# Optimization experiments

Measured on AMD Instinct MI355X. Metric: run time of the kernel, lower is better.

## Reference

```python
import jax, jax.numpy as jnp
import numpy as np

N = 8192
E = 262144
DIN = 512
DOUT = 256


def setup_inputs() -> dict:
    key = jax.random.key(0)
    k1, k2, k3, k4 = jax.random.split(key, 4)
    x = jax.random.normal(k1, (N, DIN), dtype=jnp.float32)
    edge_index = jax.random.randint(k2, (2, E), 0, N, dtype=jnp.int64)
    edge_weight = jax.random.uniform(k3, (E,), dtype=jnp.float32)
    W = jax.random.normal(k4, (DOUT, DIN), dtype=jnp.float32) * (1.0 / np.sqrt(DIN))
    return {"x": x, "edge_index": edge_index, "edge_weight": edge_weight, "W": W}


def reference(x, edge_index, edge_weight, W):
    n = x.shape[0]
    # Linear(dim_in, dim_out, bias=False): h = x @ W.T  -> [N, DOUT]
    h = x @ W.T
    # Dense adjacency: A[src, dst] += w (to_dense_adj sums duplicate edges)
    src, dst = edge_index[0], edge_index[1]
    A = jnp.zeros((n, n), dtype=x.dtype).at[src, dst].add(edge_weight)
    # degree from A BEFORE self-loops, then +1 from the added eye on degree_matrix
    deg = jnp.sum(A, axis=1) + 1.0
    # sqrt(inverse(diag(deg))) == diag(1/sqrt(deg)); apply as row scaling
    dinv_sqrt = 1.0 / jnp.sqrt(deg)  # [N]
    A = A + jnp.eye(n, dtype=x.dtype)  # self-loops on adjacency
    # x = D^{-1/2} @ (A.T @ (D^{-1/2} @ h))
    h = dinv_sqrt[:, None] * h
    h = A.T @ h
    h = dinv_sqrt[:, None] * h
    return h
```

## Files before the change

### kernel.cpp

```cpp
#include <hip/hip_runtime.h>

static constexpr int DIN = 512;
static constexpr int DOUT = 256;
static constexpr int CAP = 128;
static constexpr int EPT = 8;
static constexpr float DEG_SCALE = 1048576.0f;
static constexpr float DEG_INV = 1.0f / 1048576.0f;

typedef __attribute__((ext_vector_type(8))) short short8;
typedef __attribute__((ext_vector_type(4))) float f32x4;
typedef __attribute__((ext_vector_type(2))) unsigned int u32x2;
typedef __attribute__((ext_vector_type(4))) unsigned int u32x4;

__device__ inline unsigned short f2bf(float f) {
  unsigned int b = __float_as_uint(f);
  unsigned int r = (b + 0x7fffu + ((b >> 16) & 1u)) >> 16;
  return (unsigned short)r;
}
__device__ inline float bf_lo(unsigned int packed) { return __uint_as_float(packed << 16); }
__device__ inline float bf_hi(unsigned int packed) { return __uint_as_float(packed & 0xffff0000u); }

__device__ inline short8 cvt8(const f32x4 a, const f32x4 b) {
  short8 o;
  o[0] = (short)f2bf(a[0]); o[1] = (short)f2bf(a[1]);
  o[2] = (short)f2bf(a[2]); o[3] = (short)f2bf(a[3]);
  o[4] = (short)f2bf(b[0]); o[5] = (short)f2bf(b[1]);
  o[6] = (short)f2bf(b[2]); o[7] = (short)f2bf(b[3]);
  return o;
}

__global__ __launch_bounds__(256) void k_prep(
    const float* __restrict__ W, unsigned short* __restrict__ wbb,
    int* __restrict__ dz, int n2, int wgroups) {
  const int gid = blockIdx.x * 256 + threadIdx.x;
  if (gid < n2) dz[gid] = 0;
  const int wi = gid - n2;
  if (wi >= 0 && wi < wgroups) {
    const f32x4* src = (const f32x4*)(W + (size_t)wi * 8);
    f32x4 a = src[0], b = src[1];
    *(short8*)(wbb + (size_t)wi * 8) = cvt8(a, b);
  }
}

__global__ __launch_bounds__(256) void k_deg(
    const int* __restrict__ ei, const float* __restrict__ ew,
    int* __restrict__ degi, int E) {
  const int e0 = blockIdx.x * 256 * EPT + threadIdx.x;
  int sv[EPT], wq[EPT];
#pragma unroll
  for (int u = 0; u < EPT; ++u) {
    const int e = e0 + u * 256;
    sv[u] = __builtin_nontemporal_load(ei + e);
    wq[u] = __float2int_rn(__builtin_nontemporal_load(ew + e) * DEG_SCALE);
  }
#pragma unroll
  for (int u = 0; u < EPT; ++u) atomicAdd(&degi[sv[u]], wq[u]);
}

__global__ __launch_bounds__(256) void k_bin(
    const int* __restrict__ ei, const float* __restrict__ ew,
    int* __restrict__ cursor, uint2* __restrict__ bucket, int E) {
  const int e = blockIdx.x * 256 + threadIdx.x;
  if (e >= E) return;
  int srcv = __builtin_nontemporal_load(ei + e);
  int dstv = __builtin_nontemporal_load(ei + E + e);
  float w = __builtin_nontemporal_load(ew + e);
  int pos = atomicAdd(&cursor[dstv], 1);
  if (pos < CAP) {
    u32x2 v;
    v[0] = (unsigned)srcv;
    v[1] = __float_as_uint(w);
    __builtin_nontemporal_store(v, (u32x2*)(bucket + (size_t)dstv * CAP + pos));
  }
}

__global__ __launch_bounds__(256) void k_gemm(
    const float* __restrict__ x, const unsigned short* __restrict__ wbb,
    unsigned short* __restrict__ h1b) {
  const int lane = threadIdx.x & 63;
  const int wv = threadIdx.x >> 6;
  const int bm = blockIdx.x * 16;
  const int colb = wv * 64;
  const int r = lane & 15;
  const int kg = lane >> 4;
  f32x4 acc[4] = {};
  const float* arow = x + (size_t)(bm + r) * DIN + kg * 8;
  const unsigned short* brow0 = wbb + (size_t)(colb + r) * DIN + kg * 8;
#pragma unroll
  for (int k0 = 0; k0 < DIN; k0 += 32) {
    f32x4 a0 = *(const f32x4*)(arow + k0);
    f32x4 a1 = *(const f32x4*)(arow + k0 + 4);
    short8 av = cvt8(a0, a1);
#pragma unroll
    for (int nt = 0; nt < 4; ++nt) {
      short8 bv = *(const short8*)(brow0 + (size_t)nt * 16 * DIN + k0);
      acc[nt] = __builtin_amdgcn_mfma_f32_16x16x32_bf16(av, bv, acc[nt], 0, 0, 0);
    }
  }
#pragma unroll
  for (int i = 0; i < 4; ++i) {
    int row = bm + kg * 4 + i;
#pragma unroll
    for (int nt = 0; nt < 4; ++nt) {
      h1b[(size_t)row * DOUT + colb + nt * 16 + r] = f2bf(acc[nt][i]);
    }
  }
}

__global__ __launch_bounds__(256, 4) void k_gather(
    const unsigned short* __restrict__ h1b, const int* __restrict__ degi,
    const int* __restrict__ cursor, const uint2* __restrict__ bucket,
    float* __restrict__ out) {
  const int lane = threadIdx.x & 63;
  const int wv = threadIdx.x >> 6;
  const int dst = blockIdx.x * 4 + wv;
  const int cl = lane & 31;
  const int half = lane >> 5;
  const int cnt = min(cursor[dst], CAP);

  const u32x4 selfv = *(const u32x4*)(h1b + (size_t)dst * DOUT + cl * 8);
  const float sd = __frsqrt_rn(1.0f + (float)degi[dst] * DEG_INV);

  float acc[8] = {};

  for (int base = 0; base < cnt; base += 64) {
    const int c = min(64, cnt - base);
    int sv = 0;
    float wl = 0.f;
    if (lane < c) {
      u32x2 ev = __builtin_nontemporal_load(
          (const u32x2*)(bucket + (size_t)dst * CAP + base + lane));
      sv = (int)ev[0];
      wl = __uint_as_float(ev[1]) *
           __frsqrt_rn(1.0f + (float)degi[sv] * DEG_INV);
    }
    const int npair = ((c + 15) >> 4) << 3;
    for (int j = 0; j < npair; j += 8) {
      u32x4 rbuf[8];
#pragma unroll
      for (int u = 0; u < 8; ++u) {
        int src = __shfl(sv, 2 * (j + u) + half);
        rbuf[u] = *(const u32x4*)(h1b + (size_t)src * DOUT + cl * 8);
      }
#pragma unroll
      for (int u = 0; u < 8; ++u) {
        float w = __shfl(wl, 2 * (j + u) + half);
        acc[0] = fmaf(w, bf_lo(rbuf[u][0]), acc[0]);
        acc[1] = fmaf(w, bf_hi(rbuf[u][0]), acc[1]);
        acc[2] = fmaf(w, bf_lo(rbuf[u][1]), acc[2]);
        acc[3] = fmaf(w, bf_hi(rbuf[u][1]), acc[3]);
        acc[4] = fmaf(w, bf_lo(rbuf[u][2]), acc[4]);
        acc[5] = fmaf(w, bf_hi(rbuf[u][2]), acc[5]);
        acc[6] = fmaf(w, bf_lo(rbuf[u][3]), acc[6]);
        acc[7] = fmaf(w, bf_hi(rbuf[u][3]), acc[7]);
      }
    }
  }

#pragma unroll
  for (int k = 0; k < 8; ++k) acc[k] += __shfl_xor(acc[k], 32);

  if (half == 0) {
    f32x4 o0v, o1v;
    o0v[0] = sd * fmaf(sd, bf_lo(selfv[0]), acc[0]);
    o0v[1] = sd * fmaf(sd, bf_hi(selfv[0]), acc[1]);
    o0v[2] = sd * fmaf(sd, bf_lo(selfv[1]), acc[2]);
    o0v[3] = sd * fmaf(sd, bf_hi(selfv[1]), acc[3]);
    o1v[0] = sd * fmaf(sd, bf_lo(selfv[2]), acc[4]);
    o1v[1] = sd * fmaf(sd, bf_hi(selfv[2]), acc[5]);
    o1v[2] = sd * fmaf(sd, bf_lo(selfv[3]), acc[6]);
    o1v[3] = sd * fmaf(sd, bf_hi(selfv[3]), acc[7]);
    float* op = out + (size_t)dst * DOUT + cl * 8;
    __builtin_nontemporal_store(o0v, (f32x4*)op);
    __builtin_nontemporal_store(o1v, (f32x4*)(op + 4));
  }
}

extern "C" void kernel_launch(void* const* d_in, const int* in_sizes, int n_in,
                              void* d_out, int out_size, void* d_ws, size_t ws_size,
                              hipStream_t stream) {
  const float* x = (const float*)d_in[0];
  const int* ei = (const int*)d_in[1];
  const float* ew = (const float*)d_in[2];
  const float* W = (const float*)d_in[3];
  float* out = (float*)d_out;

  const int n = in_sizes[0] / DIN;
  const int E = in_sizes[2];

  char* p = (char*)d_ws;
  auto alloc = [&](size_t bytes) {
    char* q = p;
    p += (bytes + 255) & ~(size_t)255;
    return q;
  };
  unsigned short* h1b = (unsigned short*)alloc((size_t)n * DOUT * 2);
  unsigned short* wbb = (unsigned short*)alloc((size_t)DOUT * DIN * 2);
  int* degi    = (int*)alloc((size_t)n * 4 * 2);
  int* cursor  = degi + n;
  uint2* bucket = (uint2*)alloc((size_t)n * CAP * 8);

  const int n2 = 2 * n;
  const int wgroups = DOUT * DIN / 8;
  const int prep_blocks = (n2 + wgroups + 255) / 256;

  k_prep<<<prep_blocks, 256, 0, stream>>>(W, wbb, degi, n2, wgroups);
  k_deg<<<E / (256 * EPT), 256, 0, stream>>>(ei, ew, degi, E);
  k_bin<<<(E + 255) / 256, 256, 0, stream>>>(ei, ew, cursor, bucket, E);
  k_gemm<<<n / 16, 256, 0, stream>>>(x, wbb, h1b);
  k_gather<<<n / 4, 256, 0, stream>>>(h1b, degi, cursor, bucket, out);
}
```

Baseline: 81.01 us.

## Replicate degree and bucket counters per XCD and fuse edge kernels

Merges the degree and binning kernels into one edge pass. Atomic counters and bucket slots are replicated per XCD, with the XCD read from a hardware register, so atomics stay within one die's L2 and avoid cross-die contention. Inverse-sqrt degrees are precomputed once inside the GEMM kernel, and the gather merges the per-XCD bucket segments through a prefix sum. The risk is a per-XCD cap of 24 slots, which could drop edges for a skewed in-degree, plus extra replicas to zero and sum.

```diff
diff --git a/kernel.cpp b/kernel.cpp
--- a/kernel.cpp
+++ b/kernel.cpp
@@ -2,8 +2,9 @@
 
 static constexpr int DIN = 512;
 static constexpr int DOUT = 256;
-static constexpr int CAP = 128;
-static constexpr int EPT = 8;
+static constexpr int NR = 8;
+static constexpr int SLOT = 24;
+static constexpr int EPT = 4;
 static constexpr float DEG_SCALE = 1048576.0f;
 static constexpr float DEG_INV = 1.0f / 1048576.0f;
 
@@ -29,12 +30,18 @@
   return o;
 }
 
+__device__ inline int xcd_id() {
+  int v;
+  asm volatile("s_getreg_b32 %0, hwreg(20)" : "=s"(v));
+  return v & (NR - 1);
+}
+
 __global__ __launch_bounds__(256) void k_prep(
     const float* __restrict__ W, unsigned short* __restrict__ wbb,
-    int* __restrict__ dz, int n2, int wgroups) {
+    int* __restrict__ dz, int nz, int wgroups) {
   const int gid = blockIdx.x * 256 + threadIdx.x;
-  if (gid < n2) dz[gid] = 0;
-  const int wi = gid - n2;
+  if (gid < nz) dz[gid] = 0;
+  const int wi = gid - nz;
   if (wi >= 0 && wi < wgroups) {
     const f32x4* src = (const f32x4*)(W + (size_t)wi * 8);
     f32x4 a = src[0], b = src[1];
@@ -42,41 +49,55 @@
   }
 }
 
-__global__ __launch_bounds__(256) void k_deg(
+__global__ __launch_bounds__(256) void k_edges(
     const int* __restrict__ ei, const float* __restrict__ ew,
-    int* __restrict__ degi, int E) {
+    int* __restrict__ degi_rep, int* __restrict__ cursor_rep,
+    uint2* __restrict__ bucket, int n, int E) {
+  const int x = xcd_id();
+  int* __restrict__ degr = degi_rep + (size_t)x * n;
+  int* __restrict__ curr = cursor_rep + (size_t)x * n;
   const int e0 = blockIdx.x * 256 * EPT + threadIdx.x;
-  int sv[EPT], wq[EPT];
+  int sv[EPT], dv[EPT], wq[EPT];
+  float wf[EPT];
 #pragma unroll
   for (int u = 0; u < EPT; ++u) {
-    const int e = e0 + u * 256;
+    const int e = min(e0 + u * 256, E - 1);
     sv[u] = __builtin_nontemporal_load(ei + e);
-    wq[u] = __float2int_rn(__builtin_nontemporal_load(ew + e) * DEG_SCALE);
-  }
-#pragma unroll
-  for (int u = 0; u < EPT; ++u) atomicAdd(&degi[sv[u]], wq[u]);
-}
-
-__global__ __launch_bounds__(256) void k_bin(
-    const int* __restrict__ ei, const float* __restrict__ ew,
-    int* __restrict__ cursor, uint2* __restrict__ bucket, int E) {
-  const int e = blockIdx.x * 256 + threadIdx.x;
-  if (e >= E) return;
-  int srcv = __builtin_nontemporal_load(ei + e);
-  int dstv = __builtin_nontemporal_load(ei + E + e);
-  float w = __builtin_nontemporal_load(ew + e);
-  int pos = atomicAdd(&cursor[dstv], 1);
-  if (pos < CAP) {
-    u32x2 v;
-    v[0] = (unsigned)srcv;
-    v[1] = __float_as_uint(w);
-    __builtin_nontemporal_store(v, (u32x2*)(bucket + (size_t)dstv * CAP + pos));
+    dv[u] = __builtin_nontemporal_load(ei + E + e);
+    wf[u] = __builtin_nontemporal_load(ew + e);
+    wq[u] = __float2int_rn(wf[u] * DEG_SCALE);
+  }
+  const bool live = (e0 + (EPT - 1) * 256) < E;
+#pragma unroll
+  for (int u = 0; u < EPT; ++u)
+    if (live || e0 + u * 256 < E) atomicAdd(&degr[sv[u]], wq[u]);
+  int pos[EPT];
+#pragma unroll
+  for (int u = 0; u < EPT; ++u)
+    pos[u] = (live || e0 + u * 256 < E) ? atomicAdd(&curr[dv[u]], 1) : SLOT;
+#pragma unroll
+  for (int u = 0; u < EPT; ++u) {
+    if (pos[u] < SLOT) {
+      u32x2 v;
+      v[0] = (unsigned)sv[u];
+      v[1] = __float_as_uint(wf[u]);
+      __builtin_nontemporal_store(
+          v, (u32x2*)(bucket + ((size_t)dv[u] * NR + x) * SLOT + pos[u]));
+    }
   }
 }
 
 __global__ __launch_bounds__(256) void k_gemm(
     const float* __restrict__ x, const unsigned short* __restrict__ wbb,
-    unsigned short* __restrict__ h1b) {
+    const int* __restrict__ degi_rep, float* __restrict__ sdeg,
+    unsigned short* __restrict__ h1b, int n) {
+  if (blockIdx.x < (n >> 8)) {
+    const int i = blockIdx.x * 256 + threadIdx.x;
+    int sum = 0;
+#pragma unroll
+    for (int r = 0; r < NR; ++r) sum += degi_rep[(size_t)r * n + i];
+    sdeg[i] = __frsqrt_rn(1.0f + (float)sum * DEG_INV);
+  }
   const int lane = threadIdx.x & 63;
   const int wv = threadIdx.x >> 6;
   const int bm = blockIdx.x * 16;
@@ -108,18 +129,26 @@
 }
 
 __global__ __launch_bounds__(256, 4) void k_gather(
-    const unsigned short* __restrict__ h1b, const int* __restrict__ degi,
-    const int* __restrict__ cursor, const uint2* __restrict__ bucket,
-    float* __restrict__ out) {
+    const unsigned short* __restrict__ h1b, const float* __restrict__ sdeg,
+    const int* __restrict__ cursor_rep, const uint2* __restrict__ bucket,
+    float* __restrict__ out, int n) {
   const int lane = threadIdx.x & 63;
   const int wv = threadIdx.x >> 6;
   const int dst = blockIdx.x * 4 + wv;
   const int cl = lane & 31;
   const int half = lane >> 5;
-  const int cnt = min(cursor[dst], CAP);
+
+  int pre[NR + 1];
+  pre[0] = 0;
+#pragma unroll
+  for (int r = 0; r < NR; ++r) {
+    int c = min(cursor_rep[(size_t)r * n + dst], SLOT);
+    pre[r + 1] = pre[r] + c;
+  }
+  const int cnt = pre[NR];
 
   const u32x4 selfv = *(const u32x4*)(h1b + (size_t)dst * DOUT + cl * 8);
-  const float sd = __frsqrt_rn(1.0f + (float)degi[dst] * DEG_INV);
+  const float sd = sdeg[dst];
 
   float acc[8] = {};
 
@@ -128,11 +157,15 @@
     int sv = 0;
     float wl = 0.f;
     if (lane < c) {
+      const int g = base + lane;
+      int rr = 0;
+#pragma unroll
+      for (int r = 1; r < NR; ++r) rr += (g >= pre[r]) ? 1 : 0;
+      const int slot = g - pre[rr];
       u32x2 ev = __builtin_nontemporal_load(
-          (const u32x2*)(bucket + (size_t)dst * CAP + base + lane));
+          (const u32x2*)(bucket + ((size_t)dst * NR + rr) * SLOT + slot));
       sv = (int)ev[0];
-      wl = __uint_as_float(ev[1]) *
-           __frsqrt_rn(1.0f + (float)degi[sv] * DEG_INV);
+      wl = __uint_as_float(ev[1]) * sdeg[sv];
     }
     const int npair = ((c + 15) >> 4) << 3;
     for (int j = 0; j < npair; j += 8) {
@@ -196,17 +229,18 @@
   };
   unsigned short* h1b = (unsigned short*)alloc((size_t)n * DOUT * 2);
   unsigned short* wbb = (unsigned short*)alloc((size_t)DOUT * DIN * 2);
-  int* degi    = (int*)alloc((size_t)n * 4 * 2);
-  int* cursor  = degi + n;
-  uint2* bucket = (uint2*)alloc((size_t)n * CAP * 8);
-
-  const int n2 = 2 * n;
+  int* degi_rep   = (int*)alloc((size_t)NR * n * 4);
+  int* cursor_rep = (int*)alloc((size_t)NR * n * 4);
+  float* sdeg     = (float*)alloc((size_t)n * 4);
+  uint2* bucket   = (uint2*)alloc((size_t)n * NR * SLOT * 8);
+
+  const int nz = 2 * NR * n;
   const int wgroups = DOUT * DIN / 8;
-  const int prep_blocks = (n2 + wgroups + 255) / 256;
-
-  k_prep<<<prep_blocks, 256, 0, stream>>>(W, wbb, degi, n2, wgroups);
-  k_deg<<<E / (256 * EPT), 256, 0, stream>>>(ei, ew, degi, E);
-  k_bin<<<(E + 255) / 256, 256, 0, stream>>>(ei, ew, cursor, bucket, E);
-  k_gemm<<<n / 16, 256, 0, stream>>>(x, wbb, h1b);
-  k_gather<<<n / 4, 256, 0, stream>>>(h1b, degi, cursor, bucket, out);
-}
+  const int prep_blocks = (nz + wgroups + 255) / 256;
+  const int edge_blocks = (E + 256 * EPT - 1) / (256 * EPT);
+
+  k_prep<<<prep_blocks, 256, 0, stream>>>(W, wbb, degi_rep, nz, wgroups);
+  k_edges<<<edge_blocks, 256, 0, stream>>>(ei, ew, degi_rep, cursor_rep, bucket, n, E);
+  k_gemm<<<n / 16, 256, 0, stream>>>(x, wbb, degi_rep, sdeg, h1b, n);
+  k_gather<<<n / 4, 256, 0, stream>>>(h1b, sdeg, cursor_rep, bucket, out, n);
+}
```

Result: faster. 77.12 us (-4.8%).

## Fuse degree, binning and GEMM kernels into one block-partitioned launch

Applied to the files above, without the earlier changes.

Merges the degree-atomic kernel, the edge-binning kernel and the bf16 MFMA GEMM into one launch whose block index picks the role. The independent stages can then run at the same time on the GPU, and two launch gaps disappear. It also changes edges per thread (degree 8→4, binning 1→2) and batches the cursor atomics in the binning path. The risk is heterogeneous blocks competing for resources and uneven scheduling. The binning path also drops its E bounds check, so it relies on E being a multiple of 512.

```diff
diff --git a/kernel.cpp b/kernel.cpp
--- a/kernel.cpp
+++ b/kernel.cpp
@@ -3,7 +3,8 @@
 static constexpr int DIN = 512;
 static constexpr int DOUT = 256;
 static constexpr int CAP = 128;
-static constexpr int EPT = 8;
+static constexpr int DEPT = 4;
+static constexpr int BEPT = 2;
 static constexpr float DEG_SCALE = 1048576.0f;
 static constexpr float DEG_INV = 1.0f / 1048576.0f;
 
@@ -31,10 +32,10 @@
 
 __global__ __launch_bounds__(256) void k_prep(
     const float* __restrict__ W, unsigned short* __restrict__ wbb,
-    int* __restrict__ dz, int n2, int wgroups) {
+    int* __restrict__ dz, int nz, int wgroups) {
   const int gid = blockIdx.x * 256 + threadIdx.x;
-  if (gid < n2) dz[gid] = 0;
-  const int wi = gid - n2;
+  if (gid < nz) dz[gid] = 0;
+  const int wi = gid - nz;
   if (wi >= 0 && wi < wgroups) {
     const f32x4* src = (const f32x4*)(W + (size_t)wi * 8);
     f32x4 a = src[0], b = src[1];
@@ -42,44 +43,57 @@
   }
 }
 
-__global__ __launch_bounds__(256) void k_deg(
+__global__ __launch_bounds__(256) void k_mid(
     const int* __restrict__ ei, const float* __restrict__ ew,
-    int* __restrict__ degi, int E) {
-  const int e0 = blockIdx.x * 256 * EPT + threadIdx.x;
-  int sv[EPT], wq[EPT];
-#pragma unroll
-  for (int u = 0; u < EPT; ++u) {
-    const int e = e0 + u * 256;
-    sv[u] = __builtin_nontemporal_load(ei + e);
-    wq[u] = __float2int_rn(__builtin_nontemporal_load(ew + e) * DEG_SCALE);
-  }
-#pragma unroll
-  for (int u = 0; u < EPT; ++u) atomicAdd(&degi[sv[u]], wq[u]);
-}
-
-__global__ __launch_bounds__(256) void k_bin(
-    const int* __restrict__ ei, const float* __restrict__ ew,
-    int* __restrict__ cursor, uint2* __restrict__ bucket, int E) {
-  const int e = blockIdx.x * 256 + threadIdx.x;
-  if (e >= E) return;
-  int srcv = __builtin_nontemporal_load(ei + e);
-  int dstv = __builtin_nontemporal_load(ei + E + e);
-  float w = __builtin_nontemporal_load(ew + e);
-  int pos = atomicAdd(&cursor[dstv], 1);
-  if (pos < CAP) {
-    u32x2 v;
-    v[0] = (unsigned)srcv;
-    v[1] = __float_as_uint(w);
-    __builtin_nontemporal_store(v, (u32x2*)(bucket + (size_t)dstv * CAP + pos));
-  }
-}
-
-__global__ __launch_bounds__(256) void k_gemm(
     const float* __restrict__ x, const unsigned short* __restrict__ wbb,
-    unsigned short* __restrict__ h1b) {
+    int* __restrict__ degi, int* __restrict__ cursor,
+    uint2* __restrict__ bucket, unsigned short* __restrict__ h1b,
+    int E, int DB, int BB) {
+  const int b = blockIdx.x;
+  if (b < DB) {
+    const int e0 = b * 256 * DEPT + threadIdx.x;
+    int sv[DEPT], wq[DEPT];
+#pragma unroll
+    for (int u = 0; u < DEPT; ++u) {
+      const int e = e0 + u * 256;
+      sv[u] = __builtin_nontemporal_load(ei + e);
+      wq[u] = __float2int_rn(__builtin_nontemporal_load(ew + e) * DEG_SCALE);
+    }
+#pragma unroll
+    for (int u = 0; u < DEPT; ++u) atomicAdd(&degi[sv[u]], wq[u]);
+    return;
+  }
+  if (b < DB + BB) {
+    const int g = b - DB;
+    const int e0 = g * 256 * BEPT + threadIdx.x;
+    int sv[BEPT], dv[BEPT];
+    float wf[BEPT];
+#pragma unroll
+    for (int u = 0; u < BEPT; ++u) {
+      const int e = e0 + u * 256;
+      sv[u] = __builtin_nontemporal_load(ei + e);
+      dv[u] = __builtin_nontemporal_load(ei + E + e);
+      wf[u] = __builtin_nontemporal_load(ew + e);
+    }
+    int pos[BEPT];
+#pragma unroll
+    for (int u = 0; u < BEPT; ++u) pos[u] = atomicAdd(&cursor[dv[u]], 1);
+#pragma unroll
+    for (int u = 0; u < BEPT; ++u) {
+      if (pos[u] < CAP) {
+        u32x2 v;
+        v[0] = (unsigned)sv[u];
+        v[1] = __float_as_uint(wf[u]);
+        __builtin_nontemporal_store(
+            v, (u32x2*)(bucket + (size_t)dv[u] * CAP + pos[u]));
+      }
+    }
+    return;
+  }
+  const int g = b - DB - BB;
   const int lane = threadIdx.x & 63;
   const int wv = threadIdx.x >> 6;
-  const int bm = blockIdx.x * 16;
+  const int bm = g * 16;
   const int colb = wv * 64;
   const int r = lane & 15;
   const int kg = lane >> 4;
@@ -196,17 +210,20 @@
   };
   unsigned short* h1b = (unsigned short*)alloc((size_t)n * DOUT * 2);
   unsigned short* wbb = (unsigned short*)alloc((size_t)DOUT * DIN * 2);
-  int* degi    = (int*)alloc((size_t)n * 4 * 2);
-  int* cursor  = degi + n;
+  int* degi   = (int*)alloc((size_t)n * 4 * 2);
+  int* cursor = degi + n;
   uint2* bucket = (uint2*)alloc((size_t)n * CAP * 8);
 
-  const int n2 = 2 * n;
+  const int nz = 2 * n;
   const int wgroups = DOUT * DIN / 8;
-  const int prep_blocks = (n2 + wgroups + 255) / 256;
-
-  k_prep<<<prep_blocks, 256, 0, stream>>>(W, wbb, degi, n2, wgroups);
-  k_deg<<<E / (256 * EPT), 256, 0, stream>>>(ei, ew, degi, E);
-  k_bin<<<(E + 255) / 256, 256, 0, stream>>>(ei, ew, cursor, bucket, E);
-  k_gemm<<<n / 16, 256, 0, stream>>>(x, wbb, h1b);
+  const int prep_blocks = (nz + wgroups + 255) / 256;
+
+  const int DB = E / (256 * DEPT);
+  const int BB = E / (256 * BEPT);
+  const int GB = n / 16;
+
+  k_prep<<<prep_blocks, 256, 0, stream>>>(W, wbb, degi, nz, wgroups);
+  k_mid<<<DB + BB + GB, 256, 0, stream>>>(ei, ew, x, wbb, degi, cursor,
+                                          bucket, h1b, E, DB, BB);
   k_gather<<<n / 4, 256, 0, stream>>>(h1b, degi, cursor, bucket, out);
 }
```

Result: faster. 73.12 us (-9.7%).

## Merge prep, degree, GEMM and binning into two heterogeneous launches

Applied to the files above, without the earlier changes.

Cuts five launches down to three. The first kernel runs a privatized degree histogram in shared memory on 64 blocks alongside the GEMM blocks, and the GEMM now converts fp32 W to bf16 inline instead of using a separate prep kernel. The second kernel reduces the 64 histogram replicas into a precomputed 1/sqrt(deg) array while also binning edges, so the gather just reads sdeg. This trades global atomics and launch overhead for a 2 MB replica buffer and extra W conversion work in every GEMM block. Node count is hard-coded to 8192, and cursor zeroing must finish before binning, which the launch order guarantees.

```diff
diff --git a/kernel.cpp b/kernel.cpp
--- a/kernel.cpp
+++ b/kernel.cpp
@@ -2,8 +2,9 @@
 
 static constexpr int DIN = 512;
 static constexpr int DOUT = 256;
+static constexpr int NB = 64;
 static constexpr int CAP = 128;
-static constexpr int EPT = 8;
+static constexpr int NNODE = 8192;
 static constexpr float DEG_SCALE = 1048576.0f;
 static constexpr float DEG_INV = 1.0f / 1048576.0f;
 
@@ -29,38 +30,78 @@
   return o;
 }
 
-__global__ __launch_bounds__(256) void k_prep(
-    const float* __restrict__ W, unsigned short* __restrict__ wbb,
-    int* __restrict__ dz, int n2, int wgroups) {
-  const int gid = blockIdx.x * 256 + threadIdx.x;
-  if (gid < n2) dz[gid] = 0;
-  const int wi = gid - n2;
-  if (wi >= 0 && wi < wgroups) {
-    const f32x4* src = (const f32x4*)(W + (size_t)wi * 8);
-    f32x4 a = src[0], b = src[1];
-    *(short8*)(wbb + (size_t)wi * 8) = cvt8(a, b);
-  }
-}
-
-__global__ __launch_bounds__(256) void k_deg(
+__global__ __launch_bounds__(256) void k_d1(
     const int* __restrict__ ei, const float* __restrict__ ew,
-    int* __restrict__ degi, int E) {
-  const int e0 = blockIdx.x * 256 * EPT + threadIdx.x;
-  int sv[EPT], wq[EPT];
-#pragma unroll
-  for (int u = 0; u < EPT; ++u) {
-    const int e = e0 + u * 256;
-    sv[u] = __builtin_nontemporal_load(ei + e);
-    wq[u] = __float2int_rn(__builtin_nontemporal_load(ew + e) * DEG_SCALE);
-  }
-#pragma unroll
-  for (int u = 0; u < EPT; ++u) atomicAdd(&degi[sv[u]], wq[u]);
-}
-
-__global__ __launch_bounds__(256) void k_bin(
+    const float* __restrict__ x, const float* __restrict__ W,
+    int* __restrict__ deg_rep, int* __restrict__ cursor,
+    unsigned short* __restrict__ h1b, int E) {
+  if (blockIdx.x < NB) {
+    __shared__ int s_deg[NNODE];
+    const int b = blockIdx.x;
+    const int t = threadIdx.x;
+    for (int i = t; i < NNODE; i += 256) s_deg[i] = 0;
+    __syncthreads();
+    const int base = b * (E / NB);
+    const int iters = (E / NB) / 256;
+    for (int i = 0; i < iters; ++i) {
+      const int e = base + i * 256 + t;
+      int sv = __builtin_nontemporal_load(ei + e);
+      float w = __builtin_nontemporal_load(ew + e);
+      atomicAdd(&s_deg[sv], __float2int_rn(w * DEG_SCALE));
+    }
+    __syncthreads();
+    for (int i = t; i < NNODE; i += 256) deg_rep[b * NNODE + i] = s_deg[i];
+    return;
+  }
+  const int g = blockIdx.x - NB;
+  if (g < 32) cursor[g * 256 + threadIdx.x] = 0;
+  const int lane = threadIdx.x & 63;
+  const int wv = threadIdx.x >> 6;
+  const int bm = g * 16;
+  const int colb = wv * 64;
+  const int r = lane & 15;
+  const int kg = lane >> 4;
+  f32x4 acc[4] = {};
+  const float* arow = x + (size_t)(bm + r) * DIN + kg * 8;
+  const float* brow0 = W + (size_t)(colb + r) * DIN + kg * 8;
+#pragma unroll
+  for (int k0 = 0; k0 < DIN; k0 += 32) {
+    f32x4 a0 = *(const f32x4*)(arow + k0);
+    f32x4 a1 = *(const f32x4*)(arow + k0 + 4);
+    short8 av = cvt8(a0, a1);
+#pragma unroll
+    for (int nt = 0; nt < 4; ++nt) {
+      const float* bp = brow0 + (size_t)nt * 16 * DIN + k0;
+      f32x4 b0 = *(const f32x4*)bp;
+      f32x4 b1 = *(const f32x4*)(bp + 4);
+      short8 bv = cvt8(b0, b1);
+      acc[nt] = __builtin_amdgcn_mfma_f32_16x16x32_bf16(av, bv, acc[nt], 0, 0, 0);
+    }
+  }
+#pragma unroll
+  for (int i = 0; i < 4; ++i) {
+    int row = bm + kg * 4 + i;
+#pragma unroll
+    for (int nt = 0; nt < 4; ++nt) {
+      h1b[(size_t)row * DOUT + colb + nt * 16 + r] = f2bf(acc[nt][i]);
+    }
+  }
+}
+
+__global__ __launch_bounds__(256) void k_d2(
     const int* __restrict__ ei, const float* __restrict__ ew,
+    const int* __restrict__ deg_rep, float* __restrict__ sdeg,
     int* __restrict__ cursor, uint2* __restrict__ bucket, int E) {
-  const int e = blockIdx.x * 256 + threadIdx.x;
+  const int blk = blockIdx.x;
+  if (blk < 32) {
+    const int i = blk * 256 + threadIdx.x;
+    int sum = 0;
+#pragma unroll
+    for (int r = 0; r < NB; ++r) sum += deg_rep[r * NNODE + i];
+    sdeg[i] = __frsqrt_rn(1.0f + (float)sum * DEG_INV);
+    return;
+  }
+  const int e = (blk - 32) * 256 + threadIdx.x;
   if (e >= E) return;
   int srcv = __builtin_nontemporal_load(ei + e);
   int dstv = __builtin_nontemporal_load(ei + E + e);
@@ -74,41 +115,8 @@
   }
 }
 
-__global__ __launch_bounds__(256) void k_gemm(
-    const float* __restrict__ x, const unsigned short* __restrict__ wbb,
-    unsigned short* __restrict__ h1b) {
-  const int lane = threadIdx.x & 63;
-  const int wv = threadIdx.x >> 6;
-  const int bm = blockIdx.x * 16;
-  const int colb = wv * 64;
-  const int r = lane & 15;
-  const int kg = lane >> 4;
-  f32x4 acc[4] = {};
-  const float* arow = x + (size_t)(bm + r) * DIN + kg * 8;
-  const unsigned short* brow0 = wbb + (size_t)(colb + r) * DIN + kg * 8;
-#pragma unroll
-  for (int k0 = 0; k0 < DIN; k0 += 32) {
-    f32x4 a0 = *(const f32x4*)(arow + k0);
-    f32x4 a1 = *(const f32x4*)(arow + k0 + 4);
-    short8 av = cvt8(a0, a1);
-#pragma unroll
-    for (int nt = 0; nt < 4; ++nt) {
-      short8 bv = *(const short8*)(brow0 + (size_t)nt * 16 * DIN + k0);
-      acc[nt] = __builtin_amdgcn_mfma_f32_16x16x32_bf16(av, bv, acc[nt], 0, 0, 0);
-    }
-  }
-#pragma unroll
-  for (int i = 0; i < 4; ++i) {
-    int row = bm + kg * 4 + i;
-#pragma unroll
-    for (int nt = 0; nt < 4; ++nt) {
-      h1b[(size_t)row * DOUT + colb + nt * 16 + r] = f2bf(acc[nt][i]);
-    }
-  }
-}
-
 __global__ __launch_bounds__(256, 4) void k_gather(
-    const unsigned short* __restrict__ h1b, const int* __restrict__ degi,
+    const unsigned short* __restrict__ h1b, const float* __restrict__ sdeg,
     const int* __restrict__ cursor, const uint2* __restrict__ bucket,
     float* __restrict__ out) {
   const int lane = threadIdx.x & 63;
@@ -119,7 +127,7 @@
   const int cnt = min(cursor[dst], CAP);
 
   const u32x4 selfv = *(const u32x4*)(h1b + (size_t)dst * DOUT + cl * 8);
-  const float sd = __frsqrt_rn(1.0f + (float)degi[dst] * DEG_INV);
+  const float sd = sdeg[dst];
 
   float acc[8] = {};
 
@@ -131,8 +139,7 @@
       u32x2 ev = __builtin_nontemporal_load(
           (const u32x2*)(bucket + (size_t)dst * CAP + base + lane));
       sv = (int)ev[0];
-      wl = __uint_as_float(ev[1]) *
-           __frsqrt_rn(1.0f + (float)degi[sv] * DEG_INV);
+      wl = __uint_as_float(ev[1]) * sdeg[sv];
     }
     const int npair = ((c + 15) >> 4) << 3;
     for (int j = 0; j < npair; j += 8) {
@@ -195,18 +202,15 @@
     return q;
   };
   unsigned short* h1b = (unsigned short*)alloc((size_t)n * DOUT * 2);
-  unsigned short* wbb = (unsigned short*)alloc((size_t)DOUT * DIN * 2);
-  int* degi    = (int*)alloc((size_t)n * 4 * 2);
-  int* cursor  = degi + n;
+  int* deg_rep = (int*)alloc((size_t)NB * NNODE * 4);
+  int* cursor  = (int*)alloc((size_t)n * 4);
+  float* sdeg  = (float*)alloc((size_t)n * 4);
   uint2* bucket = (uint2*)alloc((size_t)n * CAP * 8);
 
-  const int n2 = 2 * n;
-  const int wgroups = DOUT * DIN / 8;
-  const int prep_blocks = (n2 + wgroups + 255) / 256;
-
-  k_prep<<<prep_blocks, 256, 0, stream>>>(W, wbb, degi, n2, wgroups);
-  k_deg<<<E / (256 * EPT), 256, 0, stream>>>(ei, ew, degi, E);
-  k_bin<<<(E + 255) / 256, 256, 0, stream>>>(ei, ew, cursor, bucket, E);
-  k_gemm<<<n / 16, 256, 0, stream>>>(x, wbb, h1b);
-  k_gather<<<n / 4, 256, 0, stream>>>(h1b, degi, cursor, bucket, out);
-}
+  const int GB = n / 16;
+
+  k_d1<<<NB + GB, 256, 0, stream>>>(ei, ew, x, W, deg_rep, cursor, h1b, E);
+  k_d2<<<32 + (E + 255) / 256, 256, 0, stream>>>(ei, ew, deg_rep, sdeg,
+                                                 cursor, bucket, E);
+  k_gather<<<n / 4, 256, 0, stream>>>(h1b, sdeg, cursor, bucket, out);
+}
```

New measurement: 78.37 us. 3.3% less time.
